# Optimization experiments

Hardware: AMD Instinct MI355X
Metric: run time of the kernel (lower is better)

The kernel has to match this reference:

```python
import math
import jax, jax.numpy as jnp
import numpy as np

B, T, E, H = 4, 2048, 1024, 16
D = E // H          # head_dim = 64
F = D // 2          # num_pairs = 32
FREQ_SIGMA = 1.0


def _build_spiral_frequencies(num_heads, num_pairs, freq_sigma):
    indices = np.arange(num_pairs, dtype=np.float32) + 0.5
    magnitudes = np.linspace(freq_sigma / max(num_pairs, 1), freq_sigma, num_pairs, dtype=np.float32)
    head_phases = np.linspace(0.0, 2.0 * math.pi, num_heads + 1, dtype=np.float32)[:-1][:, None]
    golden = (1.0 + math.sqrt(5.0)) / 2.0
    y = np.clip(1.0 - 2.0 * indices / float(num_pairs), -1.0, 1.0)
    radius = np.sqrt(np.clip(1.0 - y ** 2, 0.0, None))
    theta = (2.0 * math.pi * indices / golden)[None, :] + head_phases
    x = radius[None, :] * np.cos(theta)
    z = radius[None, :] * np.sin(theta)
    directions = np.stack([x, np.broadcast_to(y[None, :], (num_heads, num_pairs)), z], axis=-1)
    return (directions * magnitudes[None, :, None]).astype(np.float32)  # (H, F, 3)


def setup_inputs() -> dict:
    key = jax.random.key(0)
    ks = jax.random.split(key, 4)
    query = jax.random.normal(ks[0], (B, T, E), dtype=jnp.float32)
    positions = jax.random.normal(ks[1], (B, T, 3), dtype=jnp.float32)
    in_proj_weight = jax.random.normal(ks[2], (3 * E, E), dtype=jnp.float32) * (1.0 / math.sqrt(E))
    in_proj_bias = jnp.zeros((3 * E,), dtype=jnp.float32)
    out_proj_weight = jax.random.normal(ks[3], (E, E), dtype=jnp.float32) * (1.0 / math.sqrt(E))
    out_proj_bias = jnp.zeros((E,), dtype=jnp.float32)
    freqs = jnp.asarray(_build_spiral_frequencies(H, F, FREQ_SIGMA))
    return dict(query=query, positions=positions, in_proj_weight=in_proj_weight,
                in_proj_bias=in_proj_bias, out_proj_weight=out_proj_weight,
                out_proj_bias=out_proj_bias, freqs=freqs)


def _apply_rotary(x, positions, freqs):
    # x: (B, H, T, D), positions: (B, T, 3), freqs: (H, F, 3)
    angles = jnp.einsum('btd,hfd->bhtf', positions.astype(jnp.float32), freqs.astype(jnp.float32))
    cos = jnp.cos(angles).astype(x.dtype)
    sin = jnp.sin(angles).astype(x.dtype)
    xr = x.reshape(*x.shape[:-1], F, 2)
    x0, x1 = xr[..., 0], xr[..., 1]
    rotated = jnp.stack((x0 * cos - x1 * sin, x0 * sin + x1 * cos), axis=-1)
    return rotated.reshape(x.shape)  # rotary_dim == head_dim here


def reference(query, positions, in_proj_weight, in_proj_bias, out_proj_weight, out_proj_bias, freqs):
    b, t, e = query.shape
    h = freqs.shape[0]
    d = e // h
    # QKV projections (self-attention: all from query)
    q = query @ in_proj_weight[:e].T + in_proj_bias[:e]
    k = query @ in_proj_weight[e:2 * e].T + in_proj_bias[e:2 * e]
    v = query @ in_proj_weight[2 * e:].T + in_proj_bias[2 * e:]
    # split heads -> (B, H, T, D)
    q = q.reshape(b, t, h, d).transpose(0, 2, 1, 3)
    k = k.reshape(b, t, h, d).transpose(0, 2, 1, 3)
    v = v.reshape(b, t, h, d).transpose(0, 2, 1, 3)
    q = _apply_rotary(q, positions, freqs)
    k = _apply_rotary(k, positions, freqs)
    # SDPA
    scale = 1.0 / math.sqrt(d)
    scores = jnp.einsum('bhqd,bhkd->bhqk', q, k) * scale
    attn = jax.nn.softmax(scores, axis=-1)
    out = jnp.einsum('bhqk,bhkd->bhqd', attn, v)
    out = out.transpose(0, 2, 1, 3).reshape(b, t, e)
    return out @ out_proj_weight.T + out_proj_bias
```

## Files before the change

### kernel.cpp

```cpp
#include <hip/hip_runtime.h>
#include <math.h>

#define NB 4
#define NT 2048
#define NE 1024
#define NH 16
#define ND 64
#define NF 32

typedef _Float16 half8 __attribute__((ext_vector_type(8)));
typedef __fp16 fp16x2 __attribute__((ext_vector_type(2)));
typedef unsigned int uint2v __attribute__((ext_vector_type(2)));
typedef unsigned int uint4v __attribute__((ext_vector_type(4)));
typedef float f32x4 __attribute__((ext_vector_type(4)));
typedef float f32x16 __attribute__((ext_vector_type(16)));
#define MFMA16(a, b, c) __builtin_amdgcn_mfma_f32_16x16x32_f16(a, b, c, 0, 0, 0)
#define MFMA32(a, b, c) __builtin_amdgcn_mfma_f32_32x32x16_f16(a, b, c, 0, 0, 0)

#define GLOAD_LDS16(gsrc, ldsbase)                                            \
    __builtin_amdgcn_global_load_lds(                                         \
        (const __attribute__((address_space(1))) void*)(gsrc),                \
        (__attribute__((address_space(3))) void*)(ldsbase), 16, 0, 0)

__device__ __forceinline__ float fast_exp2(float x) {
    float r;
    asm volatile("v_exp_f32 %0, %1" : "=v"(r) : "v"(x));
    return r;
}
__device__ __forceinline__ float max3f(float a, float b, float c) {
    return fmaxf(fmaxf(a, b), c);
}

__global__ __launch_bounds__(256)
void cvt_kernel(const float* __restrict__ X, const float* __restrict__ Wi,
                const float* __restrict__ Wo,
                _Float16* __restrict__ Xh, _Float16* __restrict__ Wih,
                _Float16* __restrict__ Woh)
{
    const size_t NX = (size_t)8388608, NWI = 3145728, NWO = 1048576;
    const size_t TOT = (NX + NWI + NWO) / 8;
    for (size_t gidx = (size_t)blockIdx.x*256 + threadIdx.x; gidx < TOT;
         gidx += (size_t)gridDim.x*256) {
        size_t i = gidx*8;
        const float* src; _Float16* dst; size_t off;
        if (i < NX)            { src = X;  dst = Xh;  off = i; }
        else if (i < NX + NWI) { src = Wi; dst = Wih; off = i - NX; }
        else                   { src = Wo; dst = Woh; off = i - NX - NWI; }
        float4 a = *(const float4*)(src + off);
        float4 b = *(const float4*)(src + off + 4);
        half8 h;
        h[0]=(_Float16)a.x; h[1]=(_Float16)a.y; h[2]=(_Float16)a.z; h[3]=(_Float16)a.w;
        h[4]=(_Float16)b.x; h[5]=(_Float16)b.y; h[6]=(_Float16)b.z; h[7]=(_Float16)b.w;
        *(half8*)(dst + off) = h;
    }
}

__global__ __launch_bounds__(256)
void qkv_mfma_kernel(const _Float16* __restrict__ Ah,
                     const _Float16* __restrict__ Bh,
                     const float* __restrict__ bias,
                     const float* __restrict__ pos,
                     const float* __restrict__ freqs,
                     _Float16* __restrict__ Qh,
                     _Float16* __restrict__ Kh,
                     _Float16* __restrict__ Vh)
{
    __shared__ _Float16 Ash[128*32];
    __shared__ _Float16 Bsh[128*32];

    const int tid = threadIdx.x;
    const int wid = tid >> 6, lane = tid & 63;
    const int ln = lane & 15, g = lane >> 4;
    const int wrow = wid >> 1, wcol = wid & 1;
    const int m0 = blockIdx.x * 128, n0 = blockIdx.y * 128;

    const int r0 = tid >> 2, s0 = tid & 3;
    const int k8 = s0 ^ ((r0 >> 1) & 3);
    const _Float16* gA0 = Ah + (size_t)(m0 + r0)      * NE + k8*8;
    const _Float16* gA1 = Ah + (size_t)(m0 + r0 + 64) * NE + k8*8;
    const _Float16* gB0 = Bh + (size_t)(n0 + r0)      * NE + k8*8;
    const _Float16* gB1 = Bh + (size_t)(n0 + r0 + 64) * NE + k8*8;

    const int wb = (tid & ~63) * 8;
    _Float16* lA0 = Ash + wb;
    _Float16* lA1 = Ash + wb + 256*8;
    _Float16* lB0 = Bsh + wb;
    _Float16* lB1 = Bsh + wb + 256*8;

    const int xr = g ^ ((ln >> 1) & 3);

    f32x4 acc[4][4];
    #pragma unroll
    for (int i = 0; i < 4; ++i)
        #pragma unroll
        for (int j = 0; j < 4; ++j) acc[i][j] = (f32x4){0.f,0.f,0.f,0.f};

    for (int kt = 0; kt < NE; kt += 32) {
        if (kt) __syncthreads();
        GLOAD_LDS16(gA0 + kt, lA0);
        GLOAD_LDS16(gA1 + kt, lA1);
        GLOAD_LDS16(gB0 + kt, lB0);
        GLOAD_LDS16(gB1 + kt, lB1);
        __syncthreads();
        half8 af[4], bf[4];
        #pragma unroll
        for (int mf = 0; mf < 4; ++mf)
            af[mf] = *(const half8*)&Ash[(wrow*64 + mf*16 + ln)*32 + xr*8];
        #pragma unroll
        for (int nf = 0; nf < 4; ++nf)
            bf[nf] = *(const half8*)&Bsh[(wcol*64 + nf*16 + ln)*32 + xr*8];
        __builtin_amdgcn_s_setprio(1);
        #pragma unroll
        for (int mf = 0; mf < 4; ++mf)
            #pragma unroll
            for (int nf = 0; nf < 4; ++nf)
                acc[mf][nf] = MFMA16(af[mf], bf[nf], acc[mf][nf]);
        __builtin_amdgcn_s_setprio(0);
    }

    const int sec = n0 >> 10;
    _Float16* dst = (sec == 0) ? Qh : (sec == 1) ? Kh : Vh;

    float cb[4], fx[4], fy[4], fz[4];
    int hh[4], dd[4];
    #pragma unroll
    for (int nf = 0; nf < 4; ++nf) {
        const int col = n0 + wcol*64 + nf*16 + ln;
        cb[nf] = bias[col];
        const int e = col & 1023;
        hh[nf] = e >> 6; dd[nf] = e & 63;
        if (sec != 2) {
            const float* fq = freqs + ((size_t)hh[nf]*NF + (dd[nf] >> 1))*3;
            fx[nf] = fq[0]; fy[nf] = fq[1]; fz[nf] = fq[2];
        }
    }
    const float sgn = (ln & 1) ? 1.0f : -1.0f;
    const float qs  = (sec == 0) ? 0.125f * 1.4426950408889634f : 1.0f;

    #pragma unroll
    for (int mf = 0; mf < 4; ++mf) {
        #pragma unroll
        for (int r = 0; r < 4; ++r) {
            const int m = m0 + wrow*64 + mf*16 + g*4 + r;
            const int b = m >> 11, t = m & 2047;
            if (sec == 2) {
                #pragma unroll
                for (int nf = 0; nf < 4; ++nf)
                    dst[((size_t)(b*NH + hh[nf])*NT + t)*ND + dd[nf]] =
                        (_Float16)(acc[mf][nf][r] + cb[nf]);
            } else {
                const float px = pos[(size_t)m*3 + 0];
                const float py = pos[(size_t)m*3 + 1];
                const float pz = pos[(size_t)m*3 + 2];
                #pragma unroll
                for (int nf = 0; nf < 4; ++nf) {
                    const float x  = acc[mf][nf][r] + cb[nf];
                    const float xo = __shfl_xor(x, 1);
                    const float ang = px*fx[nf] + py*fy[nf] + pz*fz[nf];
                    float sn, cs;
                    __sincosf(ang, &sn, &cs);
                    const float out = (x*cs + sgn*xo*sn) * qs;
                    dst[((size_t)(b*NH + hh[nf])*NT + t)*ND + dd[nf]] = (_Float16)out;
                }
            }
        }
    }
}

__global__ __launch_bounds__(512, 4)
void attn_mfma_kernel(const _Float16* __restrict__ Qg, const _Float16* __restrict__ Kg,
                      const _Float16* __restrict__ Vg, _Float16* __restrict__ Og)
{
    __shared__ _Float16 Ks[2][64][70];
    __shared__ _Float16 VsT[2][64][70];

    const int tid  = threadIdx.x;
    const int wid  = tid >> 6;
    const int lane = tid & 63;
    const int m31  = lane & 31;
    const int hi   = lane >> 5;
    const int bh   = blockIdx.x;
    const int qt   = blockIdx.y;
    const int b = bh >> 4, h = bh & 15;
    const _Float16* Qp = Qg + (size_t)bh * NT * ND;
    const _Float16* Kp = Kg + (size_t)bh * NT * ND;
    const _Float16* Vp = Vg + (size_t)bh * NT * ND;

    const int qrow_g = qt*256 + wid*32 + m31;

    half8 qfr[4];
    #pragma unroll
    for (int c = 0; c < 4; ++c)
        qfr[c] = *(const half8*)(Qp + (size_t)qrow_g*ND + 16*c + 8*hi);

    f32x16 o0, o1;
    #pragma unroll
    for (int e = 0; e < 16; ++e) { o0[e] = 0.f; o1[e] = 0.f; }
    float m_i = 8.0f, l_i = 0.0f;

    const int sr  = tid >> 3;
    const int sc0 = (tid & 7) * 8;
    const int dp  = tid & 31;
    const int wv  = tid >> 5;
    const _Float16* kbase = Kp + (size_t)sr*ND + sc0;
    const _Float16* vbase = Vp + (size_t)(wv*4)*ND + 2*dp;

    half8 kv;
    unsigned int vr[4];

    #define LOADREGS(off)  do {                                              \
        kv = *(const half8*)(kbase + (size_t)(off)*ND);                      \
        _Pragma("unroll")                                                    \
        for (int j = 0; j < 4; ++j)                                          \
            vr[j] = *(const unsigned int*)(vbase + (size_t)((off) + j)*ND);  \
    } while (0)

    #define STOREBUF(bf)  do {                                               \
        *(half8*)&Ks[bf][sr][sc0] = kv;                                      \
        uint2v lod, hid;                                                     \
        lod[0] = __builtin_amdgcn_perm(vr[1], vr[0], 0x05040100u);           \
        lod[1] = __builtin_amdgcn_perm(vr[3], vr[2], 0x05040100u);           \
        hid[0] = __builtin_amdgcn_perm(vr[1], vr[0], 0x07060302u);           \
        hid[1] = __builtin_amdgcn_perm(vr[3], vr[2], 0x07060302u);           \
        *(uint2v*)&VsT[bf][2*dp][wv*4]     = lod;                            \
        *(uint2v*)&VsT[bf][2*dp + 1][wv*4] = hid;                            \
    } while (0)

    LOADREGS(0);
    STOREBUF(0);
    LOADREGS(64);

    for (int t = 0; t < 32; ++t) {
        const int cur = t & 1;
        __syncthreads();
        if (t < 31) STOREBUF(cur ^ 1);
        if (t < 30) LOADREGS((t + 2) * 64);

        f32x16 st0, st1;
        const float mneg = -m_i;
        #pragma unroll
        for (int e = 0; e < 16; ++e) { st0[e] = mneg; st1[e] = mneg; }

        __builtin_amdgcn_s_setprio(1);
        #pragma unroll
        for (int c = 0; c < 4; ++c) {
            half8 kf0 = *(const half8*)&Ks[cur][m31][16*c + 8*hi];
            half8 kf1 = *(const half8*)&Ks[cur][32 + m31][16*c + 8*hi];
            st0 = MFMA32(kf0, qfr[c], st0);
            st1 = MFMA32(kf1, qfr[c], st1);
        }
        __builtin_amdgcn_s_setprio(0);

        const fp16x2 ones2 = {(__fp16)1.0f, (__fp16)1.0f};
        unsigned int pku0[8], pku1[8];
        float rsA = 0.f, rsB = 0.f;
        float pmax = 0.f;
        #pragma unroll
        for (int j = 0; j < 8; ++j) {
            const float pa0 = fast_exp2(st0[2*j]);
            const float pa1 = fast_exp2(st0[2*j + 1]);
            const float pb0 = fast_exp2(st1[2*j]);
            const float pb1 = fast_exp2(st1[2*j + 1]);
            const fp16x2 h2a = __builtin_amdgcn_cvt_pkrtz(pa0, pa1);
            const fp16x2 h2b = __builtin_amdgcn_cvt_pkrtz(pb0, pb1);
            pku0[j] = __builtin_bit_cast(unsigned int, h2a);
            pku1[j] = __builtin_bit_cast(unsigned int, h2b);
            rsA = __builtin_amdgcn_fdot2(h2a, ones2, rsA, false);
            rsB = __builtin_amdgcn_fdot2(h2b, ones2, rsB, false);
            pmax = max3f(pmax, pa0, pa1);
            pmax = max3f(pmax, pb0, pb1);
        }
        float rs = rsA + rsB;
        rs += __shfl_xor(rs, 32);

        if (__any(pmax > 1.0f)) {
            pmax = fmaxf(pmax, __shfl_xor(pmax, 32));
            const bool  grow  = pmax > 1.0f;
            const float delta = grow ? log2f(pmax) : 0.0f;
            const float alpha = grow ? __builtin_amdgcn_rcpf(pmax) : 1.0f;
            m_i += delta;
            l_i *= alpha;
            rs  *= alpha;
            fp16x2 am; am[0] = (__fp16)alpha; am[1] = (__fp16)alpha;
            #pragma unroll
            for (int j = 0; j < 8; ++j) {
                fp16x2 p0v = __builtin_bit_cast(fp16x2, pku0[j]) * am;
                fp16x2 p1v = __builtin_bit_cast(fp16x2, pku1[j]) * am;
                pku0[j] = __builtin_bit_cast(unsigned int, p0v);
                pku1[j] = __builtin_bit_cast(unsigned int, p1v);
            }
            #pragma unroll
            for (int reg = 0; reg < 16; ++reg) {
                const int qr = (reg & 3) + 8*(reg >> 2) + 4*hi;
                const float a = __shfl(alpha, qr);
                o0[reg] *= a; o1[reg] *= a;
            }
        }
        l_i += rs;

        __builtin_amdgcn_s_setprio(1);
        #pragma unroll
        for (int kc = 0; kc < 4; ++kc) {
            const unsigned int a0 = (kc < 2) ? pku0[4*(kc & 1) + 0] : pku1[4*(kc & 1) + 0];
            const unsigned int a1 = (kc < 2) ? pku0[4*(kc & 1) + 1] : pku1[4*(kc & 1) + 1];
            const unsigned int b0 = (kc < 2) ? pku0[4*(kc & 1) + 2] : pku1[4*(kc & 1) + 2];
            const unsigned int b1 = (kc < 2) ? pku0[4*(kc & 1) + 3] : pku1[4*(kc & 1) + 3];
            uint2v rpa = __builtin_amdgcn_permlane32_swap(a0, b0, false, false);
            uint2v rpb = __builtin_amdgcn_permlane32_swap(a1, b1, false, false);
            uint4v u;
            u[0] = rpa[0]; u[1] = rpb[0]; u[2] = rpa[1]; u[3] = rpb[1];
            const half8 pa = __builtin_bit_cast(half8, u);
            const half8 vb0 = *(const half8*)&VsT[cur][m31][16*kc + 8*hi];
            const half8 vb1 = *(const half8*)&VsT[cur][32 + m31][16*kc + 8*hi];
            o0 = MFMA32(pa, vb0, o0);
            o1 = MFMA32(pa, vb1, o1);
        }
        __builtin_amdgcn_s_setprio(0);
    }

    #pragma unroll
    for (int reg = 0; reg < 16; ++reg) {
        const int qr = (reg & 3) + 8*(reg >> 2) + 4*hi;
        const float lq  = __shfl(l_i, qr);
        const float inv = 1.0f / lq;
        const int qg = qt*256 + wid*32 + qr;
        _Float16* dstp = Og + ((size_t)b*NT + qg)*NE + h*ND;
        dstp[m31]      = (_Float16)(o0[reg] * inv);
        dstp[32 + m31] = (_Float16)(o1[reg] * inv);
    }
    #undef LOADREGS
    #undef STOREBUF
}

__global__ __launch_bounds__(256)
void out_proj_mfma_kernel(const _Float16* __restrict__ Ah,
                          const _Float16* __restrict__ Bh,
                          const float* __restrict__ bias,
                          float* __restrict__ out)
{
    __shared__ _Float16 Ash[128*32];
    __shared__ _Float16 Bsh[128*32];

    const int tid = threadIdx.x;
    const int wid = tid >> 6, lane = tid & 63;
    const int ln = lane & 15, g = lane >> 4;
    const int wrow = wid >> 1, wcol = wid & 1;
    const int m0 = blockIdx.x * 128, n0 = blockIdx.y * 128;

    const int r0 = tid >> 2, s0 = tid & 3;
    const int k8 = s0 ^ ((r0 >> 1) & 3);
    const _Float16* gA0 = Ah + (size_t)(m0 + r0)      * NE + k8*8;
    const _Float16* gA1 = Ah + (size_t)(m0 + r0 + 64) * NE + k8*8;
    const _Float16* gB0 = Bh + (size_t)(n0 + r0)      * NE + k8*8;
    const _Float16* gB1 = Bh + (size_t)(n0 + r0 + 64) * NE + k8*8;

    const int wb = (tid & ~63) * 8;
    _Float16* lA0 = Ash + wb;
    _Float16* lA1 = Ash + wb + 256*8;
    _Float16* lB0 = Bsh + wb;
    _Float16* lB1 = Bsh + wb + 256*8;

    const int xr = g ^ ((ln >> 1) & 3);

    f32x4 acc[4][4];
    #pragma unroll
    for (int i = 0; i < 4; ++i)
        #pragma unroll
        for (int j = 0; j < 4; ++j) acc[i][j] = (f32x4){0.f,0.f,0.f,0.f};

    for (int kt = 0; kt < NE; kt += 32) {
        if (kt) __syncthreads();
        GLOAD_LDS16(gA0 + kt, lA0);
        GLOAD_LDS16(gA1 + kt, lA1);
        GLOAD_LDS16(gB0 + kt, lB0);
        GLOAD_LDS16(gB1 + kt, lB1);
        __syncthreads();
        half8 af[4], bf[4];
        #pragma unroll
        for (int mf = 0; mf < 4; ++mf)
            af[mf] = *(const half8*)&Ash[(wrow*64 + mf*16 + ln)*32 + xr*8];
        #pragma unroll
        for (int nf = 0; nf < 4; ++nf)
            bf[nf] = *(const half8*)&Bsh[(wcol*64 + nf*16 + ln)*32 + xr*8];
        __builtin_amdgcn_s_setprio(1);
        #pragma unroll
        for (int mf = 0; mf < 4; ++mf)
            #pragma unroll
            for (int nf = 0; nf < 4; ++nf)
                acc[mf][nf] = MFMA16(af[mf], bf[nf], acc[mf][nf]);
        __builtin_amdgcn_s_setprio(0);
    }

    float cb[4];
    #pragma unroll
    for (int nf = 0; nf < 4; ++nf) cb[nf] = bias[n0 + wcol*64 + nf*16 + ln];

    #pragma unroll
    for (int mf = 0; mf < 4; ++mf)
        #pragma unroll
        for (int r = 0; r < 4; ++r) {
            const int m = m0 + wrow*64 + mf*16 + g*4 + r;
            #pragma unroll
            for (int nf = 0; nf < 4; ++nf)
                out[(size_t)m*NE + n0 + wcol*64 + nf*16 + ln] = acc[mf][nf][r] + cb[nf];
        }
}

extern "C" void kernel_launch(void* const* d_in, const int* in_sizes, int n_in,
                              void* d_out, int out_size, void* d_ws, size_t ws_size,
                              hipStream_t stream)
{
    const float* X   = (const float*)d_in[0];
    const float* pos = (const float*)d_in[1];
    const float* Wi  = (const float*)d_in[2];
    const float* bi  = (const float*)d_in[3];
    const float* Wo  = (const float*)d_in[4];
    const float* bo  = (const float*)d_in[5];
    const float* fr  = (const float*)d_in[6];
    float* out = (float*)d_out;

    _Float16* Xh  = (_Float16*)d_ws;
    _Float16* Wih = Xh  + 8388608;
    _Float16* Woh = Wih + 3145728;
    _Float16* Qh  = Woh + 1048576;
    _Float16* Kh  = Qh  + 8388608;
    _Float16* Vh  = Kh  + 8388608;
    _Float16* Oh  = Vh  + 8388608;

    cvt_kernel          <<<3072, 256, 0, stream>>>(X, Wi, Wo, Xh, Wih, Woh);
    qkv_mfma_kernel     <<<dim3(64, 24), 256, 0, stream>>>(Xh, Wih, bi, pos, fr, Qh, Kh, Vh);
    attn_mfma_kernel    <<<dim3(64, 8), 512, 0, stream>>>(Qh, Kh, Vh, Oh);
    out_proj_mfma_kernel<<<dim3(64, 8),  256, 0, stream>>>(Oh, Woh, bo, out);
}
```

Baseline: 225.3 us.

## Double-buffer LDS tiles in QKV and output projection GEMMs

Measured after the change: 212.2 us. 5.8% less time.

```diff
diff --git a/kernel.cpp b/kernel.cpp
--- a/kernel.cpp
+++ b/kernel.cpp
@@ -65,8 +65,8 @@
                      _Float16* __restrict__ Kh,
                      _Float16* __restrict__ Vh)
 {
-    __shared__ _Float16 Ash[128*32];
-    __shared__ _Float16 Bsh[128*32];
+    __shared__ _Float16 Ash[2][128*32];
+    __shared__ _Float16 Bsh[2][128*32];
 
     const int tid = threadIdx.x;
     const int wid = tid >> 6, lane = tid & 63;
@@ -82,11 +82,6 @@
     const _Float16* gB1 = Bh + (size_t)(n0 + r0 + 64) * NE + k8*8;
 
     const int wb = (tid & ~63) * 8;
-    _Float16* lA0 = Ash + wb;
-    _Float16* lA1 = Ash + wb + 256*8;
-    _Float16* lB0 = Bsh + wb;
-    _Float16* lB1 = Bsh + wb + 256*8;
-
     const int xr = g ^ ((ln >> 1) & 3);
 
     f32x4 acc[4][4];
@@ -95,20 +90,29 @@
         #pragma unroll
         for (int j = 0; j < 4; ++j) acc[i][j] = (f32x4){0.f,0.f,0.f,0.f};
 
+    GLOAD_LDS16(gA0, Ash[0] + wb);
+    GLOAD_LDS16(gA1, Ash[0] + wb + 256*8);
+    GLOAD_LDS16(gB0, Bsh[0] + wb);
+    GLOAD_LDS16(gB1, Bsh[0] + wb + 256*8);
+    __syncthreads();
+
     for (int kt = 0; kt < NE; kt += 32) {
-        if (kt) __syncthreads();
-        GLOAD_LDS16(gA0 + kt, lA0);
-        GLOAD_LDS16(gA1 + kt, lA1);
-        GLOAD_LDS16(gB0 + kt, lB0);
-        GLOAD_LDS16(gB1 + kt, lB1);
-        __syncthreads();
+        const int cur = (kt >> 5) & 1;
+        const int nxt = cur ^ 1;
+        const int kn = kt + 32;
+        if (kn < NE) {
+            GLOAD_LDS16(gA0 + kn, Ash[nxt] + wb);
+            GLOAD_LDS16(gA1 + kn, Ash[nxt] + wb + 256*8);
+            GLOAD_LDS16(gB0 + kn, Bsh[nxt] + wb);
+            GLOAD_LDS16(gB1 + kn, Bsh[nxt] + wb + 256*8);
+        }
         half8 af[4], bf[4];
         #pragma unroll
         for (int mf = 0; mf < 4; ++mf)
-            af[mf] = *(const half8*)&Ash[(wrow*64 + mf*16 + ln)*32 + xr*8];
+            af[mf] = *(const half8*)&Ash[cur][(wrow*64 + mf*16 + ln)*32 + xr*8];
         #pragma unroll
         for (int nf = 0; nf < 4; ++nf)
-            bf[nf] = *(const half8*)&Bsh[(wcol*64 + nf*16 + ln)*32 + xr*8];
+            bf[nf] = *(const half8*)&Bsh[cur][(wcol*64 + nf*16 + ln)*32 + xr*8];
         __builtin_amdgcn_s_setprio(1);
         #pragma unroll
         for (int mf = 0; mf < 4; ++mf)
@@ -116,6 +120,7 @@
             for (int nf = 0; nf < 4; ++nf)
                 acc[mf][nf] = MFMA16(af[mf], bf[nf], acc[mf][nf]);
         __builtin_amdgcn_s_setprio(0);
+        __syncthreads();
     }
 
     const int sec = n0 >> 10;
@@ -338,8 +343,8 @@
                           const float* __restrict__ bias,
                           float* __restrict__ out)
 {
-    __shared__ _Float16 Ash[128*32];
-    __shared__ _Float16 Bsh[128*32];
+    __shared__ _Float16 Ash[2][128*32];
+    __shared__ _Float16 Bsh[2][128*32];
 
     const int tid = threadIdx.x;
     const int wid = tid >> 6, lane = tid & 63;
@@ -355,11 +360,6 @@
     const _Float16* gB1 = Bh + (size_t)(n0 + r0 + 64) * NE + k8*8;
 
     const int wb = (tid & ~63) * 8;
-    _Float16* lA0 = Ash + wb;
-    _Float16* lA1 = Ash + wb + 256*8;
-    _Float16* lB0 = Bsh + wb;
-    _Float16* lB1 = Bsh + wb + 256*8;
-
     const int xr = g ^ ((ln >> 1) & 3);
 
     f32x4 acc[4][4];
@@ -368,20 +368,29 @@
         #pragma unroll
         for (int j = 0; j < 4; ++j) acc[i][j] = (f32x4){0.f,0.f,0.f,0.f};
 
+    GLOAD_LDS16(gA0, Ash[0] + wb);
+    GLOAD_LDS16(gA1, Ash[0] + wb + 256*8);
+    GLOAD_LDS16(gB0, Bsh[0] + wb);
+    GLOAD_LDS16(gB1, Bsh[0] + wb + 256*8);
+    __syncthreads();
+
     for (int kt = 0; kt < NE; kt += 32) {
-        if (kt) __syncthreads();
-        GLOAD_LDS16(gA0 + kt, lA0);
-        GLOAD_LDS16(gA1 + kt, lA1);
-        GLOAD_LDS16(gB0 + kt, lB0);
-        GLOAD_LDS16(gB1 + kt, lB1);
-        __syncthreads();
+        const int cur = (kt >> 5) & 1;
+        const int nxt = cur ^ 1;
+        const int kn = kt + 32;
+        if (kn < NE) {
+            GLOAD_LDS16(gA0 + kn, Ash[nxt] + wb);
+            GLOAD_LDS16(gA1 + kn, Ash[nxt] + wb + 256*8);
+            GLOAD_LDS16(gB0 + kn, Bsh[nxt] + wb);
+            GLOAD_LDS16(gB1 + kn, Bsh[nxt] + wb + 256*8);
+        }
         half8 af[4], bf[4];
         #pragma unroll
         for (int mf = 0; mf < 4; ++mf)
-            af[mf] = *(const half8*)&Ash[(wrow*64 + mf*16 + ln)*32 + xr*8];
+            af[mf] = *(const half8*)&Ash[cur][(wrow*64 + mf*16 + ln)*32 + xr*8];
         #pragma unroll
         for (int nf = 0; nf < 4; ++nf)
-            bf[nf] = *(const half8*)&Bsh[(wcol*64 + nf*16 + ln)*32 + xr*8];
+            bf[nf] = *(const half8*)&Bsh[cur][(wcol*64 + nf*16 + ln)*32 + xr*8];
         __builtin_amdgcn_s_setprio(1);
         #pragma unroll
         for (int mf = 0; mf < 4; ++mf)
@@ -389,6 +398,7 @@
             for (int nf = 0; nf < 4; ++nf)
                 acc[mf][nf] = MFMA16(af[mf], bf[nf], acc[mf][nf]);
         __builtin_amdgcn_s_setprio(0);
+        __syncthreads();
     }
 
     float cb[4];
```

## Triple-buffer GEMM LDS loads and replace per-element softmax max with rowsum-triggered rescale

Applied to the files above, without the earlier changes.

New measurement: 240.8 us. 6.9% more time.

```diff
diff --git a/kernel.cpp b/kernel.cpp
--- a/kernel.cpp
+++ b/kernel.cpp
@@ -26,9 +26,6 @@
     float r;
     asm volatile("v_exp_f32 %0, %1" : "=v"(r) : "v"(x));
     return r;
-}
-__device__ __forceinline__ float max3f(float a, float b, float c) {
-    return fmaxf(fmaxf(a, b), c);
 }
 
 __global__ __launch_bounds__(256)
@@ -65,8 +62,8 @@
                      _Float16* __restrict__ Kh,
                      _Float16* __restrict__ Vh)
 {
-    __shared__ _Float16 Ash[128*32];
-    __shared__ _Float16 Bsh[128*32];
+    __shared__ _Float16 Ash[3][128*32];
+    __shared__ _Float16 Bsh[3][128*32];
 
     const int tid = threadIdx.x;
     const int wid = tid >> 6, lane = tid & 63;
@@ -82,11 +79,6 @@
     const _Float16* gB1 = Bh + (size_t)(n0 + r0 + 64) * NE + k8*8;
 
     const int wb = (tid & ~63) * 8;
-    _Float16* lA0 = Ash + wb;
-    _Float16* lA1 = Ash + wb + 256*8;
-    _Float16* lB0 = Bsh + wb;
-    _Float16* lB1 = Bsh + wb + 256*8;
-
     const int xr = g ^ ((ln >> 1) & 3);
 
     f32x4 acc[4][4];
@@ -95,28 +87,41 @@
         #pragma unroll
         for (int j = 0; j < 4; ++j) acc[i][j] = (f32x4){0.f,0.f,0.f,0.f};
 
-    for (int kt = 0; kt < NE; kt += 32) {
-        if (kt) __syncthreads();
-        GLOAD_LDS16(gA0 + kt, lA0);
-        GLOAD_LDS16(gA1 + kt, lA1);
-        GLOAD_LDS16(gB0 + kt, lB0);
-        GLOAD_LDS16(gB1 + kt, lB1);
-        __syncthreads();
-        half8 af[4], bf[4];
-        #pragma unroll
-        for (int mf = 0; mf < 4; ++mf)
-            af[mf] = *(const half8*)&Ash[(wrow*64 + mf*16 + ln)*32 + xr*8];
-        #pragma unroll
-        for (int nf = 0; nf < 4; ++nf)
-            bf[nf] = *(const half8*)&Bsh[(wcol*64 + nf*16 + ln)*32 + xr*8];
-        __builtin_amdgcn_s_setprio(1);
-        #pragma unroll
-        for (int mf = 0; mf < 4; ++mf)
-            #pragma unroll
-            for (int nf = 0; nf < 4; ++nf)
-                acc[mf][nf] = MFMA16(af[mf], bf[nf], acc[mf][nf]);
-        __builtin_amdgcn_s_setprio(0);
-    }
+    #define QKV_ISSUE(kof, buf)  do {                                        \
+        GLOAD_LDS16(gA0 + (kof), Ash[buf] + wb);                              \
+        GLOAD_LDS16(gA1 + (kof), Ash[buf] + wb + 256*8);                      \
+        GLOAD_LDS16(gB0 + (kof), Bsh[buf] + wb);                              \
+        GLOAD_LDS16(gB1 + (kof), Bsh[buf] + wb + 256*8);                      \
+    } while (0)
+
+    #define QKV_COMPUTE(buf)  do {                                            \
+        half8 af[4], bf[4];                                                   \
+        _Pragma("unroll")                                                     \
+        for (int mf = 0; mf < 4; ++mf)                                        \
+            af[mf] = *(const half8*)&Ash[buf][(wrow*64 + mf*16 + ln)*32 + xr*8]; \
+        _Pragma("unroll")                                                     \
+        for (int nf = 0; nf < 4; ++nf)                                        \
+            bf[nf] = *(const half8*)&Bsh[buf][(wcol*64 + nf*16 + ln)*32 + xr*8]; \
+        __builtin_amdgcn_s_setprio(1);                                        \
+        _Pragma("unroll")                                                     \
+        for (int mf = 0; mf < 4; ++mf)                                        \
+            _Pragma("unroll")                                                 \
+            for (int nf = 0; nf < 4; ++nf)                                    \
+                acc[mf][nf] = MFMA16(af[mf], bf[nf], acc[mf][nf]);            \
+        __builtin_amdgcn_s_setprio(0);                                        \
+    } while (0)
+
+    QKV_ISSUE(0,  0);
+    QKV_ISSUE(32, 1);
+    for (int t = 0; t < 31; ++t) {
+        asm volatile("s_waitcnt vmcnt(4)\n\ts_barrier" ::: "memory");
+        if (t + 2 < 32) QKV_ISSUE((t + 2) * 32, (t + 2) % 3);
+        QKV_COMPUTE(t % 3);
+    }
+    asm volatile("s_waitcnt vmcnt(0)\n\ts_barrier" ::: "memory");
+    QKV_COMPUTE(31 % 3);
+    #undef QKV_ISSUE
+    #undef QKV_COMPUTE
 
     const int sec = n0 >> 10;
     _Float16* dst = (sec == 0) ? Qh : (sec == 1) ? Kh : Vh;
@@ -254,40 +259,41 @@
         const fp16x2 ones2 = {(__fp16)1.0f, (__fp16)1.0f};
         unsigned int pku0[8], pku1[8];
         float rsA = 0.f, rsB = 0.f;
-        float pmax = 0.f;
-        #pragma unroll
-        for (int j = 0; j < 8; ++j) {
-            const float pa0 = fast_exp2(st0[2*j]);
-            const float pa1 = fast_exp2(st0[2*j + 1]);
-            const float pb0 = fast_exp2(st1[2*j]);
-            const float pb1 = fast_exp2(st1[2*j + 1]);
+        #pragma unroll
+        for (int jx = 0; jx < 8; ++jx) {
+            const float pa0 = fast_exp2(st0[2*jx]);
+            const float pa1 = fast_exp2(st0[2*jx + 1]);
+            const float pb0 = fast_exp2(st1[2*jx]);
+            const float pb1 = fast_exp2(st1[2*jx + 1]);
             const fp16x2 h2a = __builtin_amdgcn_cvt_pkrtz(pa0, pa1);
             const fp16x2 h2b = __builtin_amdgcn_cvt_pkrtz(pb0, pb1);
-            pku0[j] = __builtin_bit_cast(unsigned int, h2a);
-            pku1[j] = __builtin_bit_cast(unsigned int, h2b);
+            pku0[jx] = __builtin_bit_cast(unsigned int, h2a);
+            pku1[jx] = __builtin_bit_cast(unsigned int, h2b);
             rsA = __builtin_amdgcn_fdot2(h2a, ones2, rsA, false);
             rsB = __builtin_amdgcn_fdot2(h2b, ones2, rsB, false);
-            pmax = max3f(pmax, pa0, pa1);
-            pmax = max3f(pmax, pb0, pb1);
         }
         float rs = rsA + rsB;
         rs += __shfl_xor(rs, 32);
 
-        if (__any(pmax > 1.0f)) {
-            pmax = fmaxf(pmax, __shfl_xor(pmax, 32));
-            const bool  grow  = pmax > 1.0f;
-            const float delta = grow ? log2f(pmax) : 0.0f;
-            const float alpha = grow ? __builtin_amdgcn_rcpf(pmax) : 1.0f;
+        if (__any(rs > 256.0f)) {
+            float smax = st0[0];
+            #pragma unroll
+            for (int e = 1; e < 16; ++e) smax = fmaxf(smax, st0[e]);
+            #pragma unroll
+            for (int e = 0; e < 16; ++e) smax = fmaxf(smax, st1[e]);
+            smax = fmaxf(smax, __shfl_xor(smax, 32));
+            const float delta = (smax > 0.0f) ? smax : 0.0f;
+            const float alpha = fast_exp2(-delta);
             m_i += delta;
             l_i *= alpha;
             rs  *= alpha;
             fp16x2 am; am[0] = (__fp16)alpha; am[1] = (__fp16)alpha;
             #pragma unroll
-            for (int j = 0; j < 8; ++j) {
-                fp16x2 p0v = __builtin_bit_cast(fp16x2, pku0[j]) * am;
-                fp16x2 p1v = __builtin_bit_cast(fp16x2, pku1[j]) * am;
-                pku0[j] = __builtin_bit_cast(unsigned int, p0v);
-                pku1[j] = __builtin_bit_cast(unsigned int, p1v);
+            for (int jx = 0; jx < 8; ++jx) {
+                fp16x2 p0v = __builtin_bit_cast(fp16x2, pku0[jx]) * am;
+                fp16x2 p1v = __builtin_bit_cast(fp16x2, pku1[jx]) * am;
+                pku0[jx] = __builtin_bit_cast(unsigned int, p0v);
+                pku1[jx] = __builtin_bit_cast(unsigned int, p1v);
             }
             #pragma unroll
             for (int reg = 0; reg < 16; ++reg) {
@@ -338,8 +344,8 @@
                           const float* __restrict__ bias,
                           float* __restrict__ out)
 {
-    __shared__ _Float16 Ash[128*32];
-    __shared__ _Float16 Bsh[128*32];
+    __shared__ _Float16 Ash[3][128*32];
+    __shared__ _Float16 Bsh[3][128*32];
 
     const int tid = threadIdx.x;
     const int wid = tid >> 6, lane = tid & 63;
@@ -355,11 +361,6 @@
     const _Float16* gB1 = Bh + (size_t)(n0 + r0 + 64) * NE + k8*8;
 
     const int wb = (tid & ~63) * 8;
-    _Float16* lA0 = Ash + wb;
-    _Float16* lA1 = Ash + wb + 256*8;
-    _Float16* lB0 = Bsh + wb;
-    _Float16* lB1 = Bsh + wb + 256*8;
-
     const int xr = g ^ ((ln >> 1) & 3);
 
     f32x4 acc[4][4];
@@ -368,28 +369,41 @@
         #pragma unroll
         for (int j = 0; j < 4; ++j) acc[i][j] = (f32x4){0.f,0.f,0.f,0.f};
 
-    for (int kt = 0; kt < NE; kt += 32) {
-        if (kt) __syncthreads();
-        GLOAD_LDS16(gA0 + kt, lA0);
-        GLOAD_LDS16(gA1 + kt, lA1);
-        GLOAD_LDS16(gB0 + kt, lB0);
-        GLOAD_LDS16(gB1 + kt, lB1);
-        __syncthreads();
-        half8 af[4], bf[4];
-        #pragma unroll
-        for (int mf = 0; mf < 4; ++mf)
-            af[mf] = *(const half8*)&Ash[(wrow*64 + mf*16 + ln)*32 + xr*8];
-        #pragma unroll
-        for (int nf = 0; nf < 4; ++nf)
-            bf[nf] = *(const half8*)&Bsh[(wcol*64 + nf*16 + ln)*32 + xr*8];
-        __builtin_amdgcn_s_setprio(1);
-        #pragma unroll
-        for (int mf = 0; mf < 4; ++mf)
-            #pragma unroll
-            for (int nf = 0; nf < 4; ++nf)
-                acc[mf][nf] = MFMA16(af[mf], bf[nf], acc[mf][nf]);
-        __builtin_amdgcn_s_setprio(0);
-    }
+    #define OP_ISSUE(kof, buf)  do {                                         \
+        GLOAD_LDS16(gA0 + (kof), Ash[buf] + wb);                              \
+        GLOAD_LDS16(gA1 + (kof), Ash[buf] + wb + 256*8);                      \
+        GLOAD_LDS16(gB0 + (kof), Bsh[buf] + wb);                              \
+        GLOAD_LDS16(gB1 + (kof), Bsh[buf] + wb + 256*8);                      \
+    } while (0)
+
+    #define OP_COMPUTE(buf)  do {                                             \
+        half8 af[4], bf[4];                                                   \
+        _Pragma("unroll")                                                     \
+        for (int mf = 0; mf < 4; ++mf)                                        \
+            af[mf] = *(const half8*)&Ash[buf][(wrow*64 + mf*16 + ln)*32 + xr*8]; \
+        _Pragma("unroll")                                                     \
+        for (int nf = 0; nf < 4; ++nf)                                        \
+            bf[nf] = *(const half8*)&Bsh[buf][(wcol*64 + nf*16 + ln)*32 + xr*8]; \
+        __builtin_amdgcn_s_setprio(1);                                        \
+        _Pragma("unroll")                                                     \
+        for (int mf = 0; mf < 4; ++mf)                                        \
+            _Pragma("unroll")                                                 \
+            for (int nf = 0; nf < 4; ++nf)                                    \
+                acc[mf][nf] = MFMA16(af[mf], bf[nf], acc[mf][nf]);            \
+        __builtin_amdgcn_s_setprio(0);                                        \
+    } while (0)
+
+    OP_ISSUE(0,  0);
+    OP_ISSUE(32, 1);
+    for (int t = 0; t < 31; ++t) {
+        asm volatile("s_waitcnt vmcnt(4)\n\ts_barrier" ::: "memory");
+        if (t + 2 < 32) OP_ISSUE((t + 2) * 32, (t + 2) % 3);
+        OP_COMPUTE(t % 3);
+    }
+    asm volatile("s_waitcnt vmcnt(0)\n\ts_barrier" ::: "memory");
+    OP_COMPUTE(31 % 3);
+    #undef OP_ISSUE
+    #undef OP_COMPUTE
 
     float cb[4];
     #pragma unroll
```
